# Kernel tuning notes

Measured on AMD Instinct MI355X. Metric: run time of the kernel, lower is better.

## Reference

```python
import jax, jax.numpy as jnp
import numpy as np

FS = 3152
NFFT = 512
NPERSEG = 512
NOVERLAP = 341
STEP = NPERSEG - NOVERLAP  # 171
F_UP = 1500
F_LOW = 1


def _a_weight_linear(freqs):
    """10**(A(f)/10) with A(0) -> 0 weight (A(0) = -inf in the torch code)."""
    f1, f2, f3, f4 = 20.6, 107.7, 737.9, 12194.0
    A1000 = -2.0
    fsq = freqs ** 2
    num = (f4 ** 2) * freqs ** 4
    den = (fsq + f1 ** 2) * jnp.sqrt(fsq + f2 ** 2) * jnp.sqrt(fsq + f3 ** 2) * (fsq + f4 ** 2)
    A = 20.0 * jnp.log10(num / den) - A1000
    return jnp.where(freqs > 0, 10.0 ** (A / 10.0), 0.0)


def setup_inputs() -> dict:
    key = jax.random.key(0)
    x = jax.random.normal(key, (64, 262144), dtype=jnp.float32)
    return {"x": x}


def reference(x):
    B, T = x.shape
    nseg = (T - NPERSEG) // STEP + 1
    # Batched unfold via gather: [B, nseg, NPERSEG]
    idx = np.arange(nseg)[:, None] * STEP + np.arange(NPERSEG)[None, :]
    # periodic Hamming window (torch.hamming_window(periodic=True))
    window = (0.54 - 0.46 * jnp.cos(2.0 * jnp.pi * jnp.arange(NPERSEG) / NPERSEG)).astype(x.dtype)
    segs = x[:, idx] * window  # [B, nseg, 512]
    spec = jnp.fft.rfft(segs, n=NFFT, axis=-1)  # [B, nseg, 257]
    win_power = jnp.sum(window ** 2)
    psd = (spec.real ** 2 + spec.imag ** 2) / (win_power * FS)
    # one-sided correction: double all bins except DC and Nyquist
    scale = jnp.ones(NFFT // 2 + 1, dtype=x.dtype).at[1:-1].set(2.0)
    pxx = (psd * scale).mean(axis=1)  # [B, 257]

    freqs = jnp.arange(NFFT // 2 + 1, dtype=jnp.float32) * (FS / NFFT)
    aw = _a_weight_linear(freqs)  # [257]

    f_res = FS / NFFT
    lo = int(np.floor(F_LOW / f_res + 1)) - 1  # = 0
    hi = int(np.floor(F_UP / f_res + 1))       # = 244
    # 10**((10*log10(pxx)+A)/10) == pxx * 10**(A/10)
    band = jnp.sum(pxx[:, lo:hi] * aw[lo:hi], axis=1)  # [B]
    level_A = 10.0 * jnp.log10(band)
    return jnp.sum(level_A) / B
```

## Files before the change

### kernel.cpp

```cpp
#include <hip/hip_runtime.h>
#include <math.h>

#ifndef M_PI
#define M_PI 3.14159265358979323846
#endif

#define T_LEN   262144
#define NBATCH  64
#define STEP    171
#define NSEG    1531
#define NPAIR   766
#define WPB     128
#define HI_BIN  244

typedef float v2f __attribute__((ext_vector_type(2)));

__device__ __forceinline__ int bitrev3(int r) {
    return ((r & 1) << 2) | (r & 2) | ((r & 4) >> 2);
}

__device__ __forceinline__ void pswap32(float& a, float& b) {
    asm volatile("v_permlane32_swap_b32 %0, %1" : "+v"(a), "+v"(b));
}
__device__ __forceinline__ void pswap16(float& a, float& b) {
    asm volatile("v_permlane16_swap_b32 %0, %1" : "+v"(a), "+v"(b));
}
template <int CTRL>
__device__ __forceinline__ float dppf(float x) {
    return __int_as_float(__builtin_amdgcn_mov_dpp(__float_as_int(x), CTRL, 0xF, 0xF, true));
}

__device__ __forceinline__ v2f cmul(v2f z, v2f w) {
    v2f t, d;
    asm("v_pk_mul_f32 %0, %1, %2 op_sel_hi:[1,0]"
        : "=v"(t) : "v"(z), "v"(w));
    asm("v_pk_fma_f32 %0, %1, %2, %3 op_sel:[1,1,0] op_sel_hi:[0,1,1] neg_lo:[1,0,0]"
        : "=v"(d) : "v"(z), "v"(w), "v"(t));
    return d;
}
__device__ __forceinline__ v2f cmulNI(v2f z, v2f m) {
    v2f d;
    asm("v_pk_mul_f32 %0, %1, %2 op_sel:[1,0] op_sel_hi:[0,1]"
        : "=v"(d) : "v"(z), "v"(m));
    return d;
}

#define PINV(x) asm volatile("" : "+v"(x))

__global__ __launch_bounds__(256, 4) void fft_band_k(const float* __restrict__ x,
                                                     float* __restrict__ ws) {
    __shared__ __align__(16) char ldsc[4 * 4224];

    const int L      = threadIdx.x & 63;
    const int wib    = threadIdx.x >> 6;
    const int waveId = (int)(blockIdx.x * 256 + threadIdx.x) >> 6;
    const int b      = waveId >> 7;
    const int winb   = waveId & (WPB - 1);

    char* wptr = ldsc + wib * 4224 + 8 * L;
    char* rptr = ldsc + wib * 4224 + 528 * (L & 7) + 8 * (L & 0x38);

    v2f wvp[8];
#pragma unroll
    for (int r = 0; r < 8; ++r) {
        float n = (float)(L + 64 * r);
        float w = 0.54f - 0.46f * __cosf((float)(2.0 * M_PI / 512.0) * n);
        wvp[r] = (v2f){w, w};
        PINV(wvp[r]);
    }
    float wt[8];
#pragma unroll
    for (int p = 0; p < 8; ++p) {
        int k = ((L >> 2) & 1) + 2 * ((L >> 4) & 1) + 4 * ((L >> 5) & 1)
              + 8 * (L & 1) + 16 * ((L >> 1) & 1) + 32 * ((L >> 3) & 1)
              + 64 * bitrev3(p);
        int mb = (k <= 256) ? k : 512 - k;
        float wgt = 0.0f;
        if (mb >= 1 && mb < HI_BIN) {
            float f   = (float)mb * (3152.0f / 512.0f);
            float fsq = f * f;
            float num = 1.48693636e8f * fsq * fsq;
            float d1  = fsq + 424.36f;
            float d2  = fsq + 11599.29f;
            float d3  = fsq + 544496.41f;
            float d4  = fsq + 1.48693636e8f;
            float ratio = (num / (d1 * d4)) * rsqrtf(d2 * d3);
            wgt = ratio * ratio * 1.6141422e-9f;
        }
        wt[p] = wgt;
        PINV(wt[p]);
    }
    v2f M[8];
#pragma unroll
    for (int r = 1; r < 8; ++r) {
        float ang = (float)(-2.0 * M_PI / 512.0) * (float)(bitrev3(r) * L);
        float s, c; __sincosf(ang, &s, &c);
        M[r] = (v2f){c, s};
        PINV(M[r]);
    }
    float c32, s32, c16, s16;
    __sincosf((float)(-2.0 * M_PI) * (float)(L & 31) / 64.0f, &s32, &c32);
    __sincosf((float)(-2.0 * M_PI) * (float)(L & 15) / 32.0f, &s16, &c16);
    v2f W32 = (v2f){c32, s32};
    v2f W16 = (v2f){c16, s16};
    v2f W8, g8v;
    if (L & 8) { float s, c; __sincosf((float)(-2.0 * M_PI) * (float)(L & 7) / 16.0f, &s, &c);
                 W8 = (v2f){c, s}; g8v = (v2f){-1.0f, -1.0f}; }
    else       { W8 = (v2f){1.0f, 0.0f}; g8v = (v2f){1.0f, 1.0f}; }
    PINV(W32); PINV(W16); PINV(W8); PINV(g8v);

    const float C707 = 0.70710678118654752f;
    v2f W81  = (v2f){C707, -C707};
    v2f W83  = (v2f){-C707, -C707};
    v2f WNIm = (v2f){1.0f, -1.0f};
    PINV(W81); PINV(W83); PINV(WNIm);

    v2f acc2 = (v2f){0.0f, 0.0f};
    const float* xb = x + (size_t)b * T_LEN;

    for (int p = winb; p < NPAIR; p += WPB) {
        const int s0 = 2 * p;
        v2f z[8];
        const float* p0 = xb + s0 * STEP + L;
        float a[8], bb[8];
#pragma unroll
        for (int r = 0; r < 8; ++r) a[r] = p0[64 * r];
        if (2 * p + 1 < NSEG) {
#pragma unroll
            for (int r = 0; r < 8; ++r) bb[r] = p0[64 * r + STEP];
        } else {
#pragma unroll
            for (int r = 0; r < 8; ++r) bb[r] = 0.0f;
        }
#pragma unroll
        for (int r = 0; r < 8; ++r) {
            v2f zin = (v2f){a[r], bb[r]};
            z[r] = zin * wvp[r];
        }

        {
            v2f d0 = z[0] - z[4]; z[0] += z[4];
            v2f d1 = z[1] - z[5]; z[1] += z[5];
            v2f d2 = z[2] - z[6]; z[2] += z[6];
            v2f d3 = z[3] - z[7]; z[3] += z[7];
            z[4] = d0;
            z[5] = cmul(d1, W81);
            z[6] = cmulNI(d2, WNIm);
            z[7] = cmul(d3, W83);
            v2f t;
            t = z[0] - z[2]; z[0] += z[2]; z[2] = t;
            t = z[1] - z[3]; z[1] += z[3]; z[3] = cmulNI(t, WNIm);
            t = z[4] - z[6]; z[4] += z[6]; z[6] = t;
            t = z[5] - z[7]; z[5] += z[7]; z[7] = cmulNI(t, WNIm);
#pragma unroll
            for (int g = 0; g < 8; g += 2) {
                t = z[g] - z[g + 1]; z[g] += z[g + 1]; z[g + 1] = t;
            }
        }

#pragma unroll
        for (int r = 1; r < 8; ++r) z[r] = cmul(z[r], M[r]);

#pragma unroll
        for (int q = 0; q < 8; q += 2) {
            float a0 = z[q].x, a1 = z[q].y, b0 = z[q + 1].x, b1 = z[q + 1].y;
            pswap32(a0, b0); pswap32(a1, b1);
            v2f A = (v2f){a0, a1}, B = (v2f){b0, b1};
            v2f s = A + B, d = A - B;
            z[q] = s; z[q + 1] = cmul(d, W32);
        }
        {
            const int qs[4] = {0, 1, 4, 5};
#pragma unroll
            for (int t2 = 0; t2 < 4; ++t2) {
                const int q = qs[t2];
                float a0 = z[q].x, a1 = z[q].y, b0 = z[q + 2].x, b1 = z[q + 2].y;
                pswap16(a0, b0); pswap16(a1, b1);
                v2f A = (v2f){a0, a1}, B = (v2f){b0, b1};
                v2f s = A + B, d = A - B;
                z[q] = s; z[q + 2] = cmul(d, W16);
            }
        }
#pragma unroll
        for (int q = 0; q < 8; ++q) {
            v2f pp = (v2f){dppf<0x128>(z[q].x), dppf<0x128>(z[q].y)};
            v2f n = g8v * z[q] + pp;
            z[q] = cmul(n, W8);
        }

#pragma unroll
        for (int q = 0; q < 8; ++q) *(v2f*)(wptr + 528 * q) = z[q];
        v2f y[8];
#pragma unroll
        for (int q = 0; q < 8; ++q) y[q] = *(const v2f*)(rptr + 8 * q);

        {
            v2f d0 = y[0] - y[4]; y[0] += y[4];
            v2f d1 = y[1] - y[5]; y[1] += y[5];
            v2f d2 = y[2] - y[6]; y[2] += y[6];
            v2f d3 = y[3] - y[7]; y[3] += y[7];
            y[4] = d0;
            y[5] = cmul(d1, W81);
            y[6] = cmulNI(d2, WNIm);
            y[7] = cmul(d3, W83);
            v2f t;
            t = y[0] - y[2]; y[0] += y[2]; y[2] = t;
            t = y[1] - y[3]; y[1] += y[3]; y[3] = cmulNI(t, WNIm);
            t = y[4] - y[6]; y[4] += y[6]; y[6] = t;
            t = y[5] - y[7]; y[5] += y[7]; y[7] = cmulNI(t, WNIm);
#pragma unroll
            for (int g = 0; g < 8; g += 2) {
                t = y[g] - y[g + 1]; y[g] += y[g + 1]; y[g + 1] = t;
            }
        }

#pragma unroll
        for (int q = 0; q < 8; ++q) {
            v2f e = y[q] * y[q];
            acc2 += (v2f){wt[q], wt[q]} * e;
        }
    }

    float acc = acc2.x + acc2.y;
#pragma unroll
    for (int off = 32; off >= 1; off >>= 1) acc += __shfl_xor(acc, off, 64);
    if (L == 0) ws[waveId] = acc;
}

__global__ void finalize_k(const float* __restrict__ ws, float* __restrict__ out) {
    __shared__ float red[256];
    int t = threadIdx.x;
    int b = t & 63, g = t >> 6;
    float s = 0.0f;
    for (int i = 0; i < 32; ++i) s += ws[b * 128 + g * 32 + i];
    red[t] = s;
    __syncthreads();
    if (t < 64) {
        float band = red[t] + red[t + 64] + red[t + 128] + red[t + 192];
        float lv = 10.0f * log10f(band);
#pragma unroll
        for (int off = 32; off >= 1; off >>= 1) lv += __shfl_xor(lv, off, 64);
        if (t == 0) out[0] = lv * (1.0f / 64.0f);
    }
}

extern "C" void kernel_launch(void* const* d_in, const int* in_sizes, int n_in,
                              void* d_out, int out_size, void* d_ws, size_t ws_size,
                              hipStream_t stream) {
    const float* x = (const float*)d_in[0];
    float* out = (float*)d_out;
    float* ws  = (float*)d_ws;
    fft_band_k<<<(NBATCH * WPB) / 4, 256, 0, stream>>>(x, ws);
    finalize_k<<<1, 256, 0, stream>>>(ws, out);
}
```

Measured before the change: 106.5 us.

## Unroll segment-pair loop by two with double-buffered LDS and vectorized reads

The main loop now handles two segment pairs per iteration. Each pair has its own LDS buffer and its own accumulator, so the loads and FFT work of the two pairs can interleave. LDS reads become 16-byte vector loads, and the permlane asm is no longer volatile, which lets the compiler schedule it freely. The cost is double the LDS per wave and more registers, with launch bounds lowered from 4 to 3 blocks per CU, so occupancy may drop.

```diff
diff --git a/kernel.cpp b/kernel.cpp
--- a/kernel.cpp
+++ b/kernel.cpp
@@ -14,16 +14,17 @@
 #define HI_BIN  244
 
 typedef float v2f __attribute__((ext_vector_type(2)));
+typedef float v4f __attribute__((ext_vector_type(4)));
 
 __device__ __forceinline__ int bitrev3(int r) {
     return ((r & 1) << 2) | (r & 2) | ((r & 4) >> 2);
 }
 
 __device__ __forceinline__ void pswap32(float& a, float& b) {
-    asm volatile("v_permlane32_swap_b32 %0, %1" : "+v"(a), "+v"(b));
+    asm("v_permlane32_swap_b32 %0, %1" : "+v"(a), "+v"(b));
 }
 __device__ __forceinline__ void pswap16(float& a, float& b) {
-    asm volatile("v_permlane16_swap_b32 %0, %1" : "+v"(a), "+v"(b));
+    asm("v_permlane16_swap_b32 %0, %1" : "+v"(a), "+v"(b));
 }
 template <int CTRL>
 __device__ __forceinline__ float dppf(float x) {
@@ -47,9 +48,9 @@
 
 #define PINV(x) asm volatile("" : "+v"(x))
 
-__global__ __launch_bounds__(256, 4) void fft_band_k(const float* __restrict__ x,
+__global__ __launch_bounds__(256, 3) void fft_band_k(const float* __restrict__ x,
                                                      float* __restrict__ ws) {
-    __shared__ __align__(16) char ldsc[4 * 4224];
+    __shared__ __align__(16) char ldsc[4 * 8448];
 
     const int L      = threadIdx.x & 63;
     const int wib    = threadIdx.x >> 6;
@@ -57,8 +58,10 @@
     const int b      = waveId >> 7;
     const int winb   = waveId & (WPB - 1);
 
-    char* wptr = ldsc + wib * 4224 + 8 * L;
-    char* rptr = ldsc + wib * 4224 + 528 * (L & 7) + 8 * (L & 0x38);
+    char* base0 = ldsc + wib * 8448;
+    char* base1 = base0 + 4224;
+    const int woff = 8 * L;
+    const int roff = 528 * (L & 7) + 8 * (L & 0x38);
 
     v2f wvp[8];
 #pragma unroll
@@ -115,13 +118,13 @@
     v2f WNIm = (v2f){1.0f, -1.0f};
     PINV(W81); PINV(W83); PINV(WNIm);
 
-    v2f acc2 = (v2f){0.0f, 0.0f};
+    v2f accA = (v2f){0.0f, 0.0f};
+    v2f accB = (v2f){0.0f, 0.0f};
     const float* xb = x + (size_t)b * T_LEN;
 
-    for (int p = winb; p < NPAIR; p += WPB) {
-        const int s0 = 2 * p;
+    auto body = [&](int p, char* bse, v2f& acc2) __attribute__((always_inline)) {
         v2f z[8];
-        const float* p0 = xb + s0 * STEP + L;
+        const float* p0 = xb + (2 * p) * STEP + L;
         float a[8], bb[8];
 #pragma unroll
         for (int r = 0; r < 8; ++r) a[r] = p0[64 * r];
@@ -133,10 +136,7 @@
             for (int r = 0; r < 8; ++r) bb[r] = 0.0f;
         }
 #pragma unroll
-        for (int r = 0; r < 8; ++r) {
-            v2f zin = (v2f){a[r], bb[r]};
-            z[r] = zin * wvp[r];
-        }
+        for (int r = 0; r < 8; ++r) z[r] = (v2f){a[r], bb[r]} * wvp[r];
 
         {
             v2f d0 = z[0] - z[4]; z[0] += z[4];
@@ -188,11 +188,28 @@
             z[q] = cmul(n, W8);
         }
 
-#pragma unroll
-        for (int q = 0; q < 8; ++q) *(v2f*)(wptr + 528 * q) = z[q];
+        {
+            char* w0 = bse + woff;
+            char* w1 = w0 + 1056;
+            char* w2 = w0 + 2112;
+            char* w3 = w0 + 3168;
+            *(v2f*)(w0) = z[0]; *(v2f*)(w0 + 528) = z[1];
+            *(v2f*)(w1) = z[2]; *(v2f*)(w1 + 528) = z[3];
+            *(v2f*)(w2) = z[4]; *(v2f*)(w2 + 528) = z[5];
+            *(v2f*)(w3) = z[6]; *(v2f*)(w3 + 528) = z[7];
+        }
         v2f y[8];
-#pragma unroll
-        for (int q = 0; q < 8; ++q) y[q] = *(const v2f*)(rptr + 8 * q);
+        {
+            const char* rp = bse + roff;
+            v4f q0 = *(const v4f*)(rp);
+            v4f q1 = *(const v4f*)(rp + 16);
+            v4f q2 = *(const v4f*)(rp + 32);
+            v4f q3 = *(const v4f*)(rp + 48);
+            y[0] = (v2f){q0.x, q0.y}; y[1] = (v2f){q0.z, q0.w};
+            y[2] = (v2f){q1.x, q1.y}; y[3] = (v2f){q1.z, q1.w};
+            y[4] = (v2f){q2.x, q2.y}; y[5] = (v2f){q2.z, q2.w};
+            y[6] = (v2f){q3.x, q3.y}; y[7] = (v2f){q3.z, q3.w};
+        }
 
         {
             v2f d0 = y[0] - y[4]; y[0] += y[4];
@@ -219,8 +236,16 @@
             v2f e = y[q] * y[q];
             acc2 += (v2f){wt[q], wt[q]} * e;
         }
-    }
-
+    };
+
+    int p = winb;
+    for (; p + WPB < NPAIR; p += 2 * WPB) {
+        body(p, base0, accA);
+        body(p + WPB, base1, accB);
+    }
+    if (p < NPAIR) body(p, base0, accA);
+
+    v2f acc2 = accA + accB;
     float acc = acc2.x + acc2.y;
 #pragma unroll
     for (int off = 32; off >= 1; off >>= 1) acc += __shfl_xor(acc, off, 64);
```

Result: no change. 105.8 us (-0.7%).

## Run the packed FFT in fp16 with half-size LDS exchange and fdot2 power accumulation

Applied to the files above, without the earlier changes.

The whole radix-8 FFT path (twiddles, butterflies, permlane swaps, DPP exchange and LDS transpose) now uses packed half-precision complex values instead of fp32. This halves register and LDS traffic and lets one permlane/DPP op move a full complex value. Power is accumulated per bin in fp32 via fdot2, and the A-weights are applied once after the loop. The cost is a large precision loss: fp16 FFT of 512-point windows may drift from the fp32 reference, and fp16 range could be an issue for accumulated magnitudes.

```diff
diff --git a/kernel.cpp b/kernel.cpp
--- a/kernel.cpp
+++ b/kernel.cpp
@@ -13,34 +13,37 @@
 #define WPB     128
 #define HI_BIN  244
 
-typedef float v2f __attribute__((ext_vector_type(2)));
+typedef float    v2f __attribute__((ext_vector_type(2)));
+typedef _Float16 v2h __attribute__((ext_vector_type(2)));
 
 __device__ __forceinline__ int bitrev3(int r) {
     return ((r & 1) << 2) | (r & 2) | ((r & 4) >> 2);
 }
 
-__device__ __forceinline__ void pswap32(float& a, float& b) {
+__device__ __forceinline__ void pswap32h(v2h& a, v2h& b) {
     asm volatile("v_permlane32_swap_b32 %0, %1" : "+v"(a), "+v"(b));
 }
-__device__ __forceinline__ void pswap16(float& a, float& b) {
+__device__ __forceinline__ void pswap16h(v2h& a, v2h& b) {
     asm volatile("v_permlane16_swap_b32 %0, %1" : "+v"(a), "+v"(b));
 }
 template <int CTRL>
-__device__ __forceinline__ float dppf(float x) {
-    return __int_as_float(__builtin_amdgcn_mov_dpp(__float_as_int(x), CTRL, 0xF, 0xF, true));
-}
-
-__device__ __forceinline__ v2f cmul(v2f z, v2f w) {
-    v2f t, d;
-    asm("v_pk_mul_f32 %0, %1, %2 op_sel_hi:[1,0]"
+__device__ __forceinline__ v2h dpph(v2h x) {
+    int xi = __builtin_bit_cast(int, x);
+    int r  = __builtin_amdgcn_mov_dpp(xi, CTRL, 0xF, 0xF, true);
+    return __builtin_bit_cast(v2h, r);
+}
+
+__device__ __forceinline__ v2h cmulh(v2h z, v2h w) {
+    v2h t, d;
+    asm("v_pk_mul_f16 %0, %1, %2 op_sel_hi:[1,0]"
         : "=v"(t) : "v"(z), "v"(w));
-    asm("v_pk_fma_f32 %0, %1, %2, %3 op_sel:[1,1,0] op_sel_hi:[0,1,1] neg_lo:[1,0,0]"
+    asm("v_pk_fma_f16 %0, %1, %2, %3 op_sel:[1,1,0] op_sel_hi:[0,1,1] neg_lo:[1,0,0]"
         : "=v"(d) : "v"(z), "v"(w), "v"(t));
     return d;
 }
-__device__ __forceinline__ v2f cmulNI(v2f z, v2f m) {
-    v2f d;
-    asm("v_pk_mul_f32 %0, %1, %2 op_sel:[1,0] op_sel_hi:[0,1]"
+__device__ __forceinline__ v2h cmulNIh(v2h z, v2h m) {
+    v2h d;
+    asm("v_pk_mul_f16 %0, %1, %2 op_sel:[1,0] op_sel_hi:[0,1]"
         : "=v"(d) : "v"(z), "v"(m));
     return d;
 }
@@ -49,7 +52,7 @@
 
 __global__ __launch_bounds__(256, 4) void fft_band_k(const float* __restrict__ x,
                                                      float* __restrict__ ws) {
-    __shared__ __align__(16) char ldsc[4 * 4224];
+    __shared__ __align__(16) char ldsc[4 * 2080];
 
     const int L      = threadIdx.x & 63;
     const int wib    = threadIdx.x >> 6;
@@ -57,16 +60,15 @@
     const int b      = waveId >> 7;
     const int winb   = waveId & (WPB - 1);
 
-    char* wptr = ldsc + wib * 4224 + 8 * L;
-    char* rptr = ldsc + wib * 4224 + 528 * (L & 7) + 8 * (L & 0x38);
-
-    v2f wvp[8];
+    char* wptr = ldsc + wib * 2080 + 4 * L;
+    char* rptr = ldsc + wib * 2080 + 260 * (L & 7) + 4 * (L & 0x38);
+
+    float wv[8];
 #pragma unroll
     for (int r = 0; r < 8; ++r) {
         float n = (float)(L + 64 * r);
-        float w = 0.54f - 0.46f * __cosf((float)(2.0 * M_PI / 512.0) * n);
-        wvp[r] = (v2f){w, w};
-        PINV(wvp[r]);
+        wv[r] = 0.54f - 0.46f * __cosf((float)(2.0 * M_PI / 512.0) * n);
+        PINV(wv[r]);
     }
     float wt[8];
 #pragma unroll
@@ -90,37 +92,40 @@
         wt[p] = wgt;
         PINV(wt[p]);
     }
-    v2f M[8];
+    v2h M[8];
 #pragma unroll
     for (int r = 1; r < 8; ++r) {
         float ang = (float)(-2.0 * M_PI / 512.0) * (float)(bitrev3(r) * L);
         float s, c; __sincosf(ang, &s, &c);
-        M[r] = (v2f){c, s};
+        M[r] = (v2h){(_Float16)c, (_Float16)s};
         PINV(M[r]);
     }
     float c32, s32, c16, s16;
     __sincosf((float)(-2.0 * M_PI) * (float)(L & 31) / 64.0f, &s32, &c32);
     __sincosf((float)(-2.0 * M_PI) * (float)(L & 15) / 32.0f, &s16, &c16);
-    v2f W32 = (v2f){c32, s32};
-    v2f W16 = (v2f){c16, s16};
-    v2f W8, g8v;
+    v2h W32 = (v2h){(_Float16)c32, (_Float16)s32};
+    v2h W16 = (v2h){(_Float16)c16, (_Float16)s16};
+    v2h W8, g8v;
     if (L & 8) { float s, c; __sincosf((float)(-2.0 * M_PI) * (float)(L & 7) / 16.0f, &s, &c);
-                 W8 = (v2f){c, s}; g8v = (v2f){-1.0f, -1.0f}; }
-    else       { W8 = (v2f){1.0f, 0.0f}; g8v = (v2f){1.0f, 1.0f}; }
+                 W8 = (v2h){(_Float16)c, (_Float16)s}; g8v = (v2h){(_Float16)-1.f, (_Float16)-1.f}; }
+    else       { W8 = (v2h){(_Float16)1.f, (_Float16)0.f}; g8v = (v2h){(_Float16)1.f, (_Float16)1.f}; }
     PINV(W32); PINV(W16); PINV(W8); PINV(g8v);
 
-    const float C707 = 0.70710678118654752f;
-    v2f W81  = (v2f){C707, -C707};
-    v2f W83  = (v2f){-C707, -C707};
-    v2f WNIm = (v2f){1.0f, -1.0f};
+    const _Float16 C7 = (_Float16)0.70710678118654752f;
+    v2h W81  = (v2h){C7, (_Float16)-0.70710678118654752f};
+    v2h W83  = (v2h){(_Float16)-0.70710678118654752f, (_Float16)-0.70710678118654752f};
+    v2h WNIm = (v2h){(_Float16)1.f, (_Float16)-1.f};
     PINV(W81); PINV(W83); PINV(WNIm);
 
-    v2f acc2 = (v2f){0.0f, 0.0f};
+    float accQ[8];
+#pragma unroll
+    for (int q = 0; q < 8; ++q) accQ[q] = 0.0f;
+
     const float* xb = x + (size_t)b * T_LEN;
 
     for (int p = winb; p < NPAIR; p += WPB) {
         const int s0 = 2 * p;
-        v2f z[8];
+        v2h z[8];
         const float* p0 = xb + s0 * STEP + L;
         float a[8], bb[8];
 #pragma unroll
@@ -133,25 +138,23 @@
             for (int r = 0; r < 8; ++r) bb[r] = 0.0f;
         }
 #pragma unroll
-        for (int r = 0; r < 8; ++r) {
-            v2f zin = (v2f){a[r], bb[r]};
-            z[r] = zin * wvp[r];
-        }
+        for (int r = 0; r < 8; ++r)
+            z[r] = (v2h)__builtin_amdgcn_cvt_pkrtz(a[r] * wv[r], bb[r] * wv[r]);
 
         {
-            v2f d0 = z[0] - z[4]; z[0] += z[4];
-            v2f d1 = z[1] - z[5]; z[1] += z[5];
-            v2f d2 = z[2] - z[6]; z[2] += z[6];
-            v2f d3 = z[3] - z[7]; z[3] += z[7];
+            v2h d0 = z[0] - z[4]; z[0] += z[4];
+            v2h d1 = z[1] - z[5]; z[1] += z[5];
+            v2h d2 = z[2] - z[6]; z[2] += z[6];
+            v2h d3 = z[3] - z[7]; z[3] += z[7];
             z[4] = d0;
-            z[5] = cmul(d1, W81);
-            z[6] = cmulNI(d2, WNIm);
-            z[7] = cmul(d3, W83);
-            v2f t;
+            z[5] = cmulh(d1, W81);
+            z[6] = cmulNIh(d2, WNIm);
+            z[7] = cmulh(d3, W83);
+            v2h t;
             t = z[0] - z[2]; z[0] += z[2]; z[2] = t;
-            t = z[1] - z[3]; z[1] += z[3]; z[3] = cmulNI(t, WNIm);
+            t = z[1] - z[3]; z[1] += z[3]; z[3] = cmulNIh(t, WNIm);
             t = z[4] - z[6]; z[4] += z[6]; z[6] = t;
-            t = z[5] - z[7]; z[5] += z[7]; z[7] = cmulNI(t, WNIm);
+            t = z[5] - z[7]; z[5] += z[7]; z[7] = cmulNIh(t, WNIm);
 #pragma unroll
             for (int g = 0; g < 8; g += 2) {
                 t = z[g] - z[g + 1]; z[g] += z[g + 1]; z[g + 1] = t;
@@ -159,55 +162,51 @@
         }
 
 #pragma unroll
-        for (int r = 1; r < 8; ++r) z[r] = cmul(z[r], M[r]);
+        for (int r = 1; r < 8; ++r) z[r] = cmulh(z[r], M[r]);
 
 #pragma unroll
         for (int q = 0; q < 8; q += 2) {
-            float a0 = z[q].x, a1 = z[q].y, b0 = z[q + 1].x, b1 = z[q + 1].y;
-            pswap32(a0, b0); pswap32(a1, b1);
-            v2f A = (v2f){a0, a1}, B = (v2f){b0, b1};
-            v2f s = A + B, d = A - B;
-            z[q] = s; z[q + 1] = cmul(d, W32);
+            pswap32h(z[q], z[q + 1]);
+            v2h s = z[q] + z[q + 1], d = z[q] - z[q + 1];
+            z[q] = s; z[q + 1] = cmulh(d, W32);
         }
         {
             const int qs[4] = {0, 1, 4, 5};
 #pragma unroll
             for (int t2 = 0; t2 < 4; ++t2) {
                 const int q = qs[t2];
-                float a0 = z[q].x, a1 = z[q].y, b0 = z[q + 2].x, b1 = z[q + 2].y;
-                pswap16(a0, b0); pswap16(a1, b1);
-                v2f A = (v2f){a0, a1}, B = (v2f){b0, b1};
-                v2f s = A + B, d = A - B;
-                z[q] = s; z[q + 2] = cmul(d, W16);
+                pswap16h(z[q], z[q + 2]);
+                v2h s = z[q] + z[q + 2], d = z[q] - z[q + 2];
+                z[q] = s; z[q + 2] = cmulh(d, W16);
             }
         }
 #pragma unroll
         for (int q = 0; q < 8; ++q) {
-            v2f pp = (v2f){dppf<0x128>(z[q].x), dppf<0x128>(z[q].y)};
-            v2f n = g8v * z[q] + pp;
-            z[q] = cmul(n, W8);
-        }
-
-#pragma unroll
-        for (int q = 0; q < 8; ++q) *(v2f*)(wptr + 528 * q) = z[q];
-        v2f y[8];
-#pragma unroll
-        for (int q = 0; q < 8; ++q) y[q] = *(const v2f*)(rptr + 8 * q);
+            v2h pp = dpph<0x128>(z[q]);
+            v2h n  = g8v * z[q] + pp;
+            z[q] = cmulh(n, W8);
+        }
+
+#pragma unroll
+        for (int q = 0; q < 8; ++q) *(v2h*)(wptr + 260 * q) = z[q];
+        v2h y[8];
+#pragma unroll
+        for (int q = 0; q < 8; ++q) y[q] = *(volatile const v2h*)(rptr + 4 * q);
 
         {
-            v2f d0 = y[0] - y[4]; y[0] += y[4];
-            v2f d1 = y[1] - y[5]; y[1] += y[5];
-            v2f d2 = y[2] - y[6]; y[2] += y[6];
-            v2f d3 = y[3] - y[7]; y[3] += y[7];
+            v2h d0 = y[0] - y[4]; y[0] += y[4];
+            v2h d1 = y[1] - y[5]; y[1] += y[5];
+            v2h d2 = y[2] - y[6]; y[2] += y[6];
+            v2h d3 = y[3] - y[7]; y[3] += y[7];
             y[4] = d0;
-            y[5] = cmul(d1, W81);
-            y[6] = cmulNI(d2, WNIm);
-            y[7] = cmul(d3, W83);
-            v2f t;
+            y[5] = cmulh(d1, W81);
+            y[6] = cmulNIh(d2, WNIm);
+            y[7] = cmulh(d3, W83);
+            v2h t;
             t = y[0] - y[2]; y[0] += y[2]; y[2] = t;
-            t = y[1] - y[3]; y[1] += y[3]; y[3] = cmulNI(t, WNIm);
+            t = y[1] - y[3]; y[1] += y[3]; y[3] = cmulNIh(t, WNIm);
             t = y[4] - y[6]; y[4] += y[6]; y[6] = t;
-            t = y[5] - y[7]; y[5] += y[7]; y[7] = cmulNI(t, WNIm);
+            t = y[5] - y[7]; y[5] += y[7]; y[7] = cmulNIh(t, WNIm);
 #pragma unroll
             for (int g = 0; g < 8; g += 2) {
                 t = y[g] - y[g + 1]; y[g] += y[g + 1]; y[g + 1] = t;
@@ -215,13 +214,13 @@
         }
 
 #pragma unroll
-        for (int q = 0; q < 8; ++q) {
-            v2f e = y[q] * y[q];
-            acc2 += (v2f){wt[q], wt[q]} * e;
-        }
-    }
-
-    float acc = acc2.x + acc2.y;
+        for (int q = 0; q < 8; ++q)
+            accQ[q] = __builtin_amdgcn_fdot2(y[q], y[q], accQ[q], false);
+    }
+
+    float acc = 0.0f;
+#pragma unroll
+    for (int q = 0; q < 8; ++q) acc = fmaf(wt[q], accQ[q], acc);
 #pragma unroll
     for (int off = 32; off >= 1; off >>= 1) acc += __shfl_xor(acc, off, 64);
     if (L == 0) ws[waveId] = acc;
```

Result: no change. 107.6 us (+1.0%).
